# Performance work log

Measured on AMD Instinct MI355X. Metric: run time of the kernel, lower is better.

The kernel has to match this reference:

```python
import jax, jax.numpy as jnp
import numpy as np

B, T, C = 2, 2048, 2048
H, HK = 16, 4
HD = C // H
N_REP = H // HK


def setup_inputs() -> dict:
    key = jax.random.key(0)
    ks = jax.random.split(key, 10)
    sc_in = 1.0 / np.sqrt(C)
    x = jax.random.normal(ks[0], (B, T, C), dtype=jnp.float32)
    # rotary embeddings (realistic cos/sin from inv_freq)
    inv_freq = 1.0 / (10000.0 ** (jnp.arange(0, HD, 2, dtype=jnp.float32) / HD))
    freqs = jnp.arange(T, dtype=jnp.float32)[:, None] * inv_freq[None, :]  # [T, HD/2]
    emb = jnp.concatenate([freqs, freqs], axis=-1)  # [T, HD]
    cos = jnp.broadcast_to(jnp.cos(emb)[None], (B, T, HD))
    sin = jnp.broadcast_to(jnp.sin(emb)[None], (B, T, HD))
    Wq = jax.random.normal(ks[1], (C, H * HD), dtype=jnp.float32) * sc_in
    bq = jnp.zeros((H * HD,), dtype=jnp.float32)
    Wk = jax.random.normal(ks[2], (C, HK * HD), dtype=jnp.float32) * sc_in
    bk = jnp.zeros((HK * HD,), dtype=jnp.float32)
    Wv = jax.random.normal(ks[3], (C, HK * HD), dtype=jnp.float32) * sc_in
    bv = jnp.zeros((HK * HD,), dtype=jnp.float32)
    Wo = jax.random.normal(ks[4], (C, C), dtype=jnp.float32) * sc_in
    return {"x": x, "cos": cos, "sin": sin, "Wq": Wq, "bq": bq,
            "Wk": Wk, "bk": bk, "Wv": Wv, "bv": bv, "Wo": Wo}


def _rotate_half(t):
    t1, t2 = jnp.split(t, 2, axis=-1)
    return jnp.concatenate([-t2, t1], axis=-1)


def reference(x, cos, sin, Wq, bq, Wk, bk, Wv, bv, Wo):
    b, t, c = x.shape
    q = (x @ Wq + bq).reshape(b, t, H, HD).transpose(0, 2, 1, 3)   # [B,H,T,HD]
    k = (x @ Wk + bk).reshape(b, t, HK, HD).transpose(0, 2, 1, 3)  # [B,HK,T,HD]
    v = (x @ Wv + bv).reshape(b, t, HK, HD).transpose(0, 2, 1, 3)  # [B,HK,T,HD]
    co = cos[:, None, :, :]  # [B,1,T,HD]
    si = sin[:, None, :, :]
    q = q * co + _rotate_half(q) * si
    k = k * co + _rotate_half(k) * si
    # GQA without materializing repeated K/V: group query heads per KV head
    qg = q.reshape(b, HK, N_REP, t, HD)
    scale = 1.0 / np.sqrt(HD)
    scores = jnp.einsum('bgrqd,bgkd->bgrqk', qg, k) * scale  # [B,HK,n_rep,T,T]
    causal = jnp.tril(jnp.ones((t, t), dtype=bool))
    scores = jnp.where(causal, scores, jnp.finfo(scores.dtype).min)
    att = jax.nn.softmax(scores, axis=-1)
    yg = jnp.einsum('bgrqk,bgkd->bgrqd', att, v)  # [B,HK,n_rep,T,HD]
    y = yg.reshape(b, H, t, HD).transpose(0, 2, 1, 3).reshape(b, t, c)
    return y @ Wo
```

## Files before the change

kernel.cpp:

```cpp
#include <hip/hip_runtime.h>
#include <math.h>

#define BB 2
#define TT 2048
#define CC 2048
#define HH 16
#define HKK 4
#define HD 128
#define MM (BB*TT)

typedef short bf16x8 __attribute__((ext_vector_type(8)));
typedef float f32x4 __attribute__((ext_vector_type(4)));
typedef float f32x16 __attribute__((ext_vector_type(16)));
typedef int   i32x4 __attribute__((ext_vector_type(4)));

#define GLOBAL_AS(p) ((const __attribute__((address_space(1))) void*)(p))
#define LDS_AS(p)    ((__attribute__((address_space(3))) void*)(p))

__device__ __forceinline__ unsigned short f2bf(float f) {
    unsigned u = __float_as_uint(f);
    u += 0x7fff + ((u >> 16) & 1);
    return (unsigned short)(u >> 16);
}
__device__ __forceinline__ float bf2f(unsigned short h) {
    return __uint_as_float(((unsigned)h) << 16);
}

#define QSCALE (0.08838834764831845f * 1.44269504088896340736f)

__global__ __launch_bounds__(256) void prep_kernel(
    const float* __restrict__ x, const float* __restrict__ Wq,
    const float* __restrict__ Wk, const float* __restrict__ Wv,
    const float* __restrict__ Wo, unsigned short* __restrict__ xb,
    unsigned short* __restrict__ Wt, unsigned short* __restrict__ Wot)
{
    __shared__ float tile[64][65];
    int z = blockIdx.z;
    if (z >= 4) {
        int bid = (z - 4) * 1024 + blockIdx.y * 32 + blockIdx.x;
        size_t i = ((size_t)bid * 256 + threadIdx.x) * 8;
        float4 a = *(const float4*)&x[i];
        float4 b = *(const float4*)&x[i + 4];
        uint4 r;
        r.x = f2bf(a.x) | ((unsigned)f2bf(a.y) << 16);
        r.y = f2bf(a.z) | ((unsigned)f2bf(a.w) << 16);
        r.z = f2bf(b.x) | ((unsigned)f2bf(b.y) << 16);
        r.w = f2bf(b.z) | ((unsigned)f2bf(b.w) << 16);
        *(uint4*)&xb[i] = r;
        return;
    }
    const float* src; unsigned short* dst; int ldW, nmax, noff;
    if (z == 0)      { src = Wq; dst = Wt;  ldW = 2048; nmax = 2048; noff = 0; }
    else if (z == 1) { src = Wk; dst = Wt;  ldW = 512;  nmax = 512;  noff = 2048; }
    else if (z == 2) { src = Wv; dst = Wt;  ldW = 512;  nmax = 512;  noff = 2560; }
    else             { src = Wo; dst = Wot; ldW = 2048; nmax = 2048; noff = 0; }
    int n0 = blockIdx.y * 64;
    if (n0 >= nmax) return;
    int k0 = blockIdx.x * 64;
    int tx = threadIdx.x & 15, ty = threadIdx.x >> 4;
#pragma unroll
    for (int i = 0; i < 4; ++i) {
        int r = ty + i * 16;
        float4 v4 = *(const float4*)&src[(size_t)(k0 + r) * ldW + n0 + tx * 4];
        tile[r][tx * 4 + 0] = v4.x;
        tile[r][tx * 4 + 1] = v4.y;
        tile[r][tx * 4 + 2] = v4.z;
        tile[r][tx * 4 + 3] = v4.w;
    }
    __syncthreads();
#pragma unroll
    for (int i = 0; i < 4; ++i) {
        int r = ty + i * 16;
        int c = tx * 4;
        ushort4 o;
        o.x = f2bf(tile[c + 0][r]);
        o.y = f2bf(tile[c + 1][r]);
        o.z = f2bf(tile[c + 2][r]);
        o.w = f2bf(tile[c + 3][r]);
        *(ushort4*)&dst[(size_t)(noff + n0 + r) * 2048 + k0 + c] = o;
    }
}

__device__ __forceinline__ void gemm_core_128x128x64(
    const unsigned short* __restrict__ A, const unsigned short* __restrict__ B,
    short* As, short* Bs, int m0, int n0,
    const int* mrow, const int* nrow, f32x4 (&acc)[4][4])
{
    const int tid = threadIdx.x;
    const int lane = tid & 63;
    const int w = tid >> 6;
    const int lm = lane & 15;
    const int q8 = lane >> 4;
    const int lrow = lane >> 3;
    const int lchunk = lane & 7;

    for (int kt = 0; kt < CC; kt += 64) {
        __syncthreads();
#pragma unroll
        for (int jj = 0; jj < 4; ++jj) {
            int rA = w * 32 + jj * 8 + lrow;
            int cA = ((lchunk ^ (rA & 7)) << 3);
            __builtin_amdgcn_global_load_lds(
                GLOBAL_AS(&A[(size_t)(m0 + rA) * CC + kt + cA]),
                LDS_AS(&As[(w * 32 + jj * 8) * 64]), 16, 0, 0);
            __builtin_amdgcn_global_load_lds(
                GLOBAL_AS(&B[(size_t)(n0 + rA) * CC + kt + cA]),
                LDS_AS(&Bs[(w * 32 + jj * 8) * 64]), 16, 0, 0);
        }
        __syncthreads();
#pragma unroll
        for (int ksi = 0; ksi < 2; ++ksi) {
            bf16x8 af[4], bfr[4];
#pragma unroll
            for (int i = 0; i < 4; ++i) {
                int xo = (((ksi * 4 + q8) ^ (lm & 7)) << 3);
                af[i]  = *(const bf16x8*)&As[(mrow[i] + lm) * 64 + xo];
                bfr[i] = *(const bf16x8*)&Bs[(nrow[i] + lm) * 64 + xo];
            }
#pragma unroll
            for (int im = 0; im < 4; ++im)
#pragma unroll
                for (int in = 0; in < 4; ++in)
                    acc[im][in] = __builtin_amdgcn_mfma_f32_16x16x32_bf16(af[im], bfr[in], acc[im][in], 0, 0, 0);
        }
    }
}

__global__ __launch_bounds__(256, 3) void qkv_gemm_mfma(
    const unsigned short* __restrict__ xb, const unsigned short* __restrict__ Wt,
    const float* __restrict__ bq, const float* __restrict__ bk, const float* __restrict__ bv,
    const float* __restrict__ cosb, const float* __restrict__ sinb,
    unsigned short* __restrict__ q, unsigned short* __restrict__ k, unsigned short* __restrict__ v)
{
    __shared__ __attribute__((aligned(16))) short As[128 * 64];
    __shared__ __attribute__((aligned(16))) short Bs[128 * 64];
    const int lane = threadIdx.x & 63;
    const int w = threadIdx.x >> 6;
    const int w1 = w >> 1;
    const int m0 = blockIdx.y * 128;
    const int n0 = blockIdx.x * 128;
    const int lm = lane & 15;
    const int q8 = lane >> 4;

    int mrow[4], nrow[4];
#pragma unroll
    for (int i = 0; i < 4; ++i) {
        mrow[i] = (w & 1) * 64 + i * 16;
        nrow[i] = w1 * 32 + (i & 1) * 16 + (i >> 1) * 64;
    }

    f32x4 acc[4][4];
#pragma unroll
    for (int im = 0; im < 4; ++im)
#pragma unroll
        for (int in = 0; in < 4; ++in) acc[im][in] = {0.f, 0.f, 0.f, 0.f};

    gemm_core_128x128x64(xb, Wt, As, Bs, m0, n0, mrow, nrow, acc);

    unsigned short* dst; const float* bias; int ldD, off, mode;
    if (n0 < 2048)      { dst = q; bias = bq; ldD = 2048; off = n0;        mode = 0; }
    else if (n0 < 2560) { dst = k; bias = bk; ldD = 512;  off = n0 - 2048; mode = 1; }
    else                { dst = v; bias = bv; ldD = 512;  off = n0 - 2560; mode = 2; }

    float bv_[4];
#pragma unroll
    for (int in = 0; in < 4; ++in) bv_[in] = bias[off + nrow[in] + lm];

#pragma unroll
    for (int im = 0; im < 4; ++im) {
        int rowbase = m0 + mrow[im] + q8 * 4;
        float t[4][4];
#pragma unroll
        for (int in = 0; in < 4; ++in)
#pragma unroll
            for (int r = 0; r < 4; ++r) t[in][r] = acc[im][in][r] + bv_[in];
        if (mode < 2) {
#pragma unroll
            for (int in = 0; in < 4; ++in) {
                int d = nrow[in] + lm;
                float sgn = (in < 2) ? -1.f : 1.f;
#pragma unroll
                for (int r = 0; r < 4; ++r) {
                    int row = rowbase + r;
                    float c = cosb[row * HD + d];
                    float s = sinb[row * HD + d];
                    float o = c * t[in][r] + sgn * s * t[in ^ 2][r];
                    if (mode == 0) o *= QSCALE;
                    dst[(size_t)row * ldD + off + d] = f2bf(o);
                }
            }
        } else {
#pragma unroll
            for (int in = 0; in < 4; ++in)
#pragma unroll
                for (int r = 0; r < 4; ++r)
                    dst[(size_t)(rowbase + r) * ldD + off + nrow[in] + lm] = f2bf(t[in][r]);
        }
    }
}

__global__ __launch_bounds__(256, 3) void out_gemm_mfma(
    const unsigned short* __restrict__ yb, const unsigned short* __restrict__ Wot,
    float* __restrict__ Cout)
{
    __shared__ __attribute__((aligned(16))) short As[128 * 64];
    __shared__ __attribute__((aligned(16))) short Bs[128 * 64];
    const int lane = threadIdx.x & 63;
    const int w = threadIdx.x >> 6;
    const int m0 = blockIdx.y * 128;
    const int n0 = blockIdx.x * 128;
    const int lm = lane & 15;
    const int q8 = lane >> 4;

    int mrow[4], nrow[4];
#pragma unroll
    for (int i = 0; i < 4; ++i) {
        mrow[i] = (w & 1) * 64 + i * 16;
        nrow[i] = (w >> 1) * 64 + i * 16;
    }

    f32x4 acc[4][4];
#pragma unroll
    for (int im = 0; im < 4; ++im)
#pragma unroll
        for (int in = 0; in < 4; ++in) acc[im][in] = {0.f, 0.f, 0.f, 0.f};

    gemm_core_128x128x64(yb, Wot, As, Bs, m0, n0, mrow, nrow, acc);

#pragma unroll
    for (int im = 0; im < 4; ++im)
#pragma unroll
        for (int in = 0; in < 4; ++in)
#pragma unroll
            for (int r = 0; r < 4; ++r) {
                int row = m0 + mrow[im] + q8 * 4 + r;
                Cout[(size_t)row * CC + n0 + nrow[in] + lm] = acc[im][in][r];
            }
}

__global__ __launch_bounds__(256) void vtrans_kernel(
    const unsigned short* __restrict__ v, unsigned short* __restrict__ vt)
{
    __shared__ unsigned short tile[64][68];
    int bg = blockIdx.z;
    int b = bg >> 2, g = bg & 3;
    int t0 = blockIdx.x * 64;
    int d0 = blockIdx.y * 64;
    int tx = threadIdx.x & 15, ty = threadIdx.x >> 4;
#pragma unroll
    for (int i = 0; i < 4; ++i) {
        int r = ty + i * 16;
        ushort4 v4 = *(const ushort4*)&v[(size_t)(b * TT + t0 + r) * (HKK * HD) + g * HD + d0 + tx * 4];
        tile[r][tx * 4 + 0] = v4.x;
        tile[r][tx * 4 + 1] = v4.y;
        tile[r][tx * 4 + 2] = v4.z;
        tile[r][tx * 4 + 3] = v4.w;
    }
    __syncthreads();
#pragma unroll
    for (int i = 0; i < 4; ++i) {
        int r = ty + i * 16;
        int c = tx * 4;
        ushort4 o;
        o.x = tile[c + 0][r];
        o.y = tile[c + 1][r];
        o.z = tile[c + 2][r];
        o.w = tile[c + 3][r];
        *(ushort4*)&vt[(size_t)(bg * HD + d0 + r) * TT + t0 + c] = o;
    }
}

static __device__ const signed char QI_T[24] = {
    15, 7, 14, 14, 13, 6, 12, 11,
    15, 13, 12, 10, 10, 9, 11, 5,
    0, 1, 2, 3, 8, 4, 8, 9
};
static __device__ const signed char HF_T[24] = {
    0, 2, 0, 1, 1, 2, 1, 1,
    1, 0, 0, 0, 1, 0, 0, 2,
    2, 2, 2, 2, 0, 2, 1, 1
};

__global__ __launch_bounds__(256, 3) void flash_mfma(
    const unsigned short* __restrict__ q, const unsigned short* __restrict__ k,
    const unsigned short* __restrict__ vt, unsigned short* __restrict__ y,
    float* __restrict__ po, float* __restrict__ sb)
{
    __shared__ __attribute__((aligned(16))) short SM[24576];
    short* Vs = SM + 16384;

    const int tid = threadIdx.x;
    const int lane = tid & 63;
    const int w = tid >> 6;
    const int l31 = lane & 31;
    const int hi = lane >> 5;
    const int swz = (l31 & 7) << 3;
    const int bh = blockIdx.x;
    const int b = bh >> 4, h = bh & 15, g = h >> 2;
    const int yb_ = blockIdx.y;
    const int qi = QI_T[yb_];
    const int hf = HF_T[yb_];
    const int q0 = qi * 128;
    const int jdiag = 2 * qi + (w >> 1);
    int j0, jend;
    if (hf == 2)      { j0 = 0;      jend = 2 * qi + 2; }
    else if (hf == 0) { j0 = 0;      jend = qi + 1; }
    else              { j0 = qi + 1; jend = 2 * qi + 2; }

    bf16x8 qf[8];
#pragma unroll
    for (int ks = 0; ks < 8; ++ks)
        qf[ks] = *(const bf16x8*)&q[(size_t)(b * TT + q0 + w * 32 + l31) * CC
                                    + h * HD + ks * 16 + hi * 8];

    f32x16 o_acc[4];
#pragma unroll
    for (int t = 0; t < 4; ++t)
#pragma unroll
        for (int e = 0; e < 16; ++e) o_acc[t][e] = 0.f;
    float m_i = -1e30f;
    float l_i = 0.f;

    const unsigned short* kbase = k + (size_t)(b * TT) * (HKK * HD) + g * HD;
    const unsigned short* vbase = vt + (size_t)((b * 4 + g) * HD) * TT;
    int ko[4], vo[4];
#pragma unroll
    for (int i = 0; i < 4; ++i) {
        int c = (i * 4 + w) * 64 + lane;
        int kt_ = c >> 4, kc = c & 15;
        ko[i] = kt_ * (HKK * HD) + ((kc ^ (kt_ & 7)) << 3);
        int dv = c >> 3, vc = c & 7;
        vo[i] = dv * TT + ((vc ^ (dv & 7)) << 3);
    }

#define STAGE_K(cb, jj) do {                                                 \
    short* Kd = SM + (cb) * 8192;                                            \
    _Pragma("unroll")                                                        \
    for (int i_ = 0; i_ < 4; ++i_)                                           \
        __builtin_amdgcn_global_load_lds(                                    \
            GLOBAL_AS(kbase + (size_t)(jj) * 64 * (HKK * HD) + ko[i_]),      \
            LDS_AS(Kd + (i_ * 4 + w) * 512), 16, 0, 0);                      \
} while (0)
#define STAGE_V(jj) do {                                                     \
    _Pragma("unroll")                                                        \
    for (int i_ = 0; i_ < 4; ++i_)                                           \
        __builtin_amdgcn_global_load_lds(                                    \
            GLOBAL_AS(vbase + (size_t)(jj) * 64 + vo[i_]),                   \
            LDS_AS(Vs + (i_ * 4 + w) * 512), 16, 0, 0);                      \
} while (0)

    STAGE_K(0, j0);
    __syncthreads();

    int c = 0;
    for (int j = j0; j < jend; ++j) {
        STAGE_V(j);
        int jn = (j + 1 < jend) ? j + 1 : j;
        STAGE_K(c ^ 1, jn);

        f32x16 sacc[2];
        if (j <= jdiag) {
            const short* Ks = SM + c * 8192;
#pragma unroll
            for (int ct = 0; ct < 2; ++ct) {
#pragma unroll
                for (int e = 0; e < 16; ++e) sacc[ct][e] = 0.f;
#pragma unroll
                for (int ks = 0; ks < 8; ++ks) {
                    bf16x8 kf = *(const bf16x8*)&Ks[(ct * 32 + l31) * 128
                                                    + (((2 * ks + hi) << 3) ^ swz)];
                    sacc[ct] = __builtin_amdgcn_mfma_f32_32x32x16_bf16(kf, qf[ks], sacc[ct], 0, 0, 0);
                }
            }
            if (j == jdiag) {
                int lim = l31 + 32 * (w & 1);
#pragma unroll
                for (int ct = 0; ct < 2; ++ct)
#pragma unroll
                    for (int reg = 0; reg < 16; ++reg) {
                        int tok = ct * 32 + (reg & 3) + 8 * (reg >> 2) + 4 * hi;
                        if (tok > lim) sacc[ct][reg] = -1e30f;
                    }
            }
            float mx[8];
#pragma unroll
            for (int e = 0; e < 8; ++e)
                mx[e] = fmaxf(fmaxf(sacc[0][e], sacc[0][e + 8]),
                              fmaxf(sacc[1][e], sacc[1][e + 8]));
            float tmax = fmaxf(fmaxf(fmaxf(mx[0], mx[1]), fmaxf(mx[2], mx[3])),
                               fmaxf(fmaxf(mx[4], mx[5]), fmaxf(mx[6], mx[7])));
            tmax = fmaxf(tmax, __shfl_xor(tmax, 32));
            float m_new = fmaxf(m_i, tmax);
            float alpha = exp2f(m_i - m_new);
            m_i = m_new;

#pragma unroll
            for (int ct = 0; ct < 2; ++ct)
#pragma unroll
                for (int e = 0; e < 16; ++e)
                    sacc[ct][e] = exp2f(sacc[ct][e] - m_new);
            float s8[8];
#pragma unroll
            for (int e = 0; e < 8; ++e)
                s8[e] = (sacc[0][e] + sacc[0][e + 8]) + (sacc[1][e] + sacc[1][e + 8]);
            float ps = ((s8[0] + s8[1]) + (s8[2] + s8[3]))
                     + ((s8[4] + s8[5]) + (s8[6] + s8[7]));
            l_i = l_i * alpha + ps;

#pragma unroll
            for (int t = 0; t < 4; ++t)
#pragma unroll
                for (int e = 0; e < 16; ++e) o_acc[t][e] *= alpha;
        }

        asm volatile("s_waitcnt vmcnt(4)" ::: "memory");
        __builtin_amdgcn_sched_barrier(0);
        __builtin_amdgcn_s_barrier();
        __builtin_amdgcn_sched_barrier(0);

        if (j <= jdiag) {
#pragma unroll
            for (int ks = 0; ks < 4; ++ks) {
                const int ct = ks >> 1, base = 8 * (ks & 1);
                int a0, a1, b0, b1;
                asm("v_cvt_pk_bf16_f32 %0, %1, %2" : "=v"(a0)
                    : "v"(sacc[ct][base + 0]), "v"(sacc[ct][base + 1]));
                asm("v_cvt_pk_bf16_f32 %0, %1, %2" : "=v"(a1)
                    : "v"(sacc[ct][base + 2]), "v"(sacc[ct][base + 3]));
                asm("v_cvt_pk_bf16_f32 %0, %1, %2" : "=v"(b0)
                    : "v"(sacc[ct][base + 4]), "v"(sacc[ct][base + 5]));
                asm("v_cvt_pk_bf16_f32 %0, %1, %2" : "=v"(b1)
                    : "v"(sacc[ct][base + 6]), "v"(sacc[ct][base + 7]));
                asm("v_permlane32_swap_b32 %0, %1" : "+v"(a0), "+v"(b0));
                asm("v_permlane32_swap_b32 %0, %1" : "+v"(a1), "+v"(b1));
                i32x4 wv; wv[0] = a0; wv[1] = a1; wv[2] = b0; wv[3] = b1;
                bf16x8 pa = __builtin_bit_cast(bf16x8, wv);
#pragma unroll
                for (int t = 0; t < 4; ++t) {
                    bf16x8 vf = *(const bf16x8*)&Vs[(t * 32 + l31) * 64
                                                    + (((2 * ks + hi) << 3) ^ swz)];
                    o_acc[t] = __builtin_amdgcn_mfma_f32_32x32x16_bf16(vf, pa, o_acc[t], 0, 0, 0);
                }
            }
        }

        __syncthreads();
        c ^= 1;
    }
#undef STAGE_K
#undef STAGE_V

    float lf = l_i + __shfl_xor(l_i, 32);
    float invl = 1.f / lf;

    if (hf == 2) {
        short* Es = SM;
#pragma unroll
        for (int t = 0; t < 4; ++t)
#pragma unroll
            for (int rg = 0; rg < 4; ++rg) {
                ushort4 o;
                o.x = f2bf(o_acc[t][rg * 4 + 0] * invl);
                o.y = f2bf(o_acc[t][rg * 4 + 1] * invl);
                o.z = f2bf(o_acc[t][rg * 4 + 2] * invl);
                o.w = f2bf(o_acc[t][rg * 4 + 3] * invl);
                *(ushort4*)&Es[(w * 32 + l31) * 136 + t * 32 + 8 * rg + 4 * hi] = o;
            }
        __syncthreads();
#pragma unroll
        for (int i = 0; i < 8; ++i) {
            int f = tid + i * 256;
            int row = f >> 4, ch = f & 15;
            uint4 tv = *(const uint4*)&Es[row * 136 + ch * 8];
            *(uint4*)&y[(size_t)(b * TT + q0 + row) * CC + h * HD + ch * 8] = tv;
        }
    } else {
        const int pi = ((bh << 3) + (qi - 8)) * 2 + hf;
        if (hi == 0) sb[pi * 128 + w * 32 + l31] = lf * exp2f(m_i);
        float* pb = po + (size_t)pi * 16384;
#pragma unroll
        for (int t = 0; t < 4; ++t)
#pragma unroll
            for (int rg = 0; rg < 4; ++rg) {
                float4 o;
                o.x = o_acc[t][rg * 4 + 0] * invl;
                o.y = o_acc[t][rg * 4 + 1] * invl;
                o.z = o_acc[t][rg * 4 + 2] * invl;
                o.w = o_acc[t][rg * 4 + 3] * invl;
                *(float4*)&pb[(w * 32 + l31) * 128 + t * 32 + 8 * rg + 4 * hi] = o;
            }
    }
}

__global__ __launch_bounds__(256) void combine_kernel(
    const float* __restrict__ po, const float* __restrict__ sb,
    unsigned short* __restrict__ y)
{
    const int bh = blockIdx.x;
    const int b = bh >> 4, h = bh & 15;
    const int qi = 8 + blockIdx.y;
    const int p0 = ((bh << 3) + (qi - 8)) * 2;
    const int t = threadIdx.x;
    const int row = t >> 1, d0 = (t & 1) * 64;
    float s0 = sb[p0 * 128 + row];
    float s1 = sb[(p0 + 1) * 128 + row];
    float w0 = s0 / (s0 + s1);
    float w1 = 1.f - w0;
    const float* a = &po[(size_t)p0 * 16384 + row * 128 + d0];
    const float* c = &po[(size_t)(p0 + 1) * 16384 + row * 128 + d0];
    unsigned short* yr = &y[(size_t)(b * TT + qi * 128 + row) * CC + h * HD + d0];
#pragma unroll
    for (int i = 0; i < 64; i += 4) {
        float4 xa = *(const float4*)&a[i];
        float4 xc = *(const float4*)&c[i];
        ushort4 o;
        o.x = f2bf(w0 * xa.x + w1 * xc.x);
        o.y = f2bf(w0 * xa.y + w1 * xc.y);
        o.z = f2bf(w0 * xa.z + w1 * xc.z);
        o.w = f2bf(w0 * xa.w + w1 * xc.w);
        *(ushort4*)&yr[i] = o;
    }
}

extern "C" void kernel_launch(void* const* d_in, const int* in_sizes, int n_in,
                              void* d_out, int out_size, void* d_ws, size_t ws_size,
                              hipStream_t stream) {
    const float* x    = (const float*)d_in[0];
    const float* cosb = (const float*)d_in[1];
    const float* sinb = (const float*)d_in[2];
    const float* Wq   = (const float*)d_in[3];
    const float* bq   = (const float*)d_in[4];
    const float* Wk   = (const float*)d_in[5];
    const float* bk   = (const float*)d_in[6];
    const float* Wv   = (const float*)d_in[7];
    const float* bv   = (const float*)d_in[8];
    const float* Wo   = (const float*)d_in[9];
    float* out = (float*)d_out;

    unsigned short* xb  = (unsigned short*)d_ws;
    unsigned short* Wt  = xb  + (size_t)MM * CC;
    unsigned short* Wot = Wt  + (size_t)3072 * 2048;
    unsigned short* qb  = Wot + (size_t)2048 * 2048;
    unsigned short* kb  = qb  + (size_t)MM * CC;
    unsigned short* vb  = kb  + (size_t)MM * (HKK * HD);
    unsigned short* vtb = vb  + (size_t)MM * (HKK * HD);
    unsigned short* ybf = vtb + (size_t)BB * HKK * HD * TT;

    float* po = (float*)d_out;
    float* sbuf = (float*)xb;

    prep_kernel<<<dim3(32, 32, 8), 256, 0, stream>>>(x, Wq, Wk, Wv, Wo, xb, Wt, Wot);
    qkv_gemm_mfma<<<dim3(3072 / 128, MM / 128), 256, 0, stream>>>(
        xb, Wt, bq, bk, bv, cosb, sinb, qb, kb, vb);
    vtrans_kernel<<<dim3(TT / 64, HD / 64, BB * HKK), 256, 0, stream>>>(vb, vtb);
    flash_mfma<<<dim3(BB * HH, 24), 256, 0, stream>>>(qb, kb, vtb, ybf, po, sbuf);
    combine_kernel<<<dim3(BB * HH, 8), 256, 0, stream>>>(po, sbuf, ybf);
    out_gemm_mfma<<<dim3(CC / 128, MM / 128), 256, 0, stream>>>(ybf, Wot, out);
}
```

Measured before the change: 312.7 us.

## Fuse V transpose into QKV GEMM, swizzle GEMM blocks, lazy softmax rescale

The QKV GEMM epilogue for V tiles now transposes through LDS and writes the transposed V layout directly, so the separate vtrans kernel and its launch go away. Both GEMMs remap block indices with an XCD-aware swizzle to improve L2 locality. The flash kernel skips the running-max rescale of the output accumulator when the new tile max stays within a threshold of the old one (the FA4-style lazy rescale), and raises wave priority around the MFMA sections. The added LDS buffer for the transpose may reduce occupancy, and the lazy rescale lets exponentials exceed 1 by up to 2^8, which bounds their range but slightly changes numerics.

```diff
diff --git a/kernel.cpp b/kernel.cpp
--- a/kernel.cpp
+++ b/kernel.cpp
@@ -21,9 +21,6 @@
     unsigned u = __float_as_uint(f);
     u += 0x7fff + ((u >> 16) & 1);
     return (unsigned short)(u >> 16);
-}
-__device__ __forceinline__ float bf2f(unsigned short h) {
-    return __uint_as_float(((unsigned)h) << 16);
 }
 
 #define QSCALE (0.08838834764831845f * 1.44269504088896340736f)
@@ -130,15 +127,22 @@
     const unsigned short* __restrict__ xb, const unsigned short* __restrict__ Wt,
     const float* __restrict__ bq, const float* __restrict__ bk, const float* __restrict__ bv,
     const float* __restrict__ cosb, const float* __restrict__ sinb,
-    unsigned short* __restrict__ q, unsigned short* __restrict__ k, unsigned short* __restrict__ v)
+    unsigned short* __restrict__ q, unsigned short* __restrict__ k,
+    unsigned short* __restrict__ vt)
 {
-    __shared__ __attribute__((aligned(16))) short As[128 * 64];
-    __shared__ __attribute__((aligned(16))) short Bs[128 * 64];
-    const int lane = threadIdx.x & 63;
-    const int w = threadIdx.x >> 6;
+    __shared__ __attribute__((aligned(16))) short SM[17408];
+    short* As = SM;
+    short* Bs = SM + 8192;
+    const int tid = threadIdx.x;
+    const int lane = tid & 63;
+    const int w = tid >> 6;
     const int w1 = w >> 1;
-    const int m0 = blockIdx.y * 128;
-    const int n0 = blockIdx.x * 128;
+    const int nx = gridDim.x;
+    const int nwg = nx * gridDim.y;
+    const int bid = blockIdx.y * nx + blockIdx.x;
+    const int swb = (bid & 7) * (nwg >> 3) + (bid >> 3);
+    const int m0 = (swb / nx) * 128;
+    const int n0 = (swb % nx) * 128;
     const int lm = lane & 15;
     const int q8 = lane >> 4;
 
@@ -160,11 +164,47 @@
     unsigned short* dst; const float* bias; int ldD, off, mode;
     if (n0 < 2048)      { dst = q; bias = bq; ldD = 2048; off = n0;        mode = 0; }
     else if (n0 < 2560) { dst = k; bias = bk; ldD = 512;  off = n0 - 2048; mode = 1; }
-    else                { dst = v; bias = bv; ldD = 512;  off = n0 - 2560; mode = 2; }
+    else                { dst = 0; bias = bv; ldD = 0;    off = n0 - 2560; mode = 2; }
 
     float bv_[4];
 #pragma unroll
     for (int in = 0; in < 4; ++in) bv_[in] = bias[off + nrow[in] + lm];
+
+    if (mode == 2) {
+        __syncthreads();
+        short* Ts = SM;
+#pragma unroll
+        for (int im = 0; im < 4; ++im) {
+            int rowb = mrow[im] + q8 * 4;
+#pragma unroll
+            for (int in = 0; in < 4; ++in) {
+                float bvv = bv_[in];
+#pragma unroll
+                for (int r = 0; r < 4; ++r)
+                    Ts[(rowb + r) * 136 + nrow[in] + lm] =
+                        (short)f2bf(acc[im][in][r] + bvv);
+            }
+        }
+        __syncthreads();
+        int d = tid >> 1, th = (tid & 1) * 64;
+        int bb = m0 >> 11, t0 = m0 & 2047, gg = off >> 7;
+        unsigned short* vr = &vt[(size_t)((bb * 4 + gg) * HD + d) * TT + t0 + th];
+#pragma unroll
+        for (int i = 0; i < 8; ++i) {
+            int tb = th + i * 8;
+            unsigned o0 = (unsigned short)Ts[(tb + 0) * 136 + d]
+                        | ((unsigned)(unsigned short)Ts[(tb + 1) * 136 + d] << 16);
+            unsigned o1 = (unsigned short)Ts[(tb + 2) * 136 + d]
+                        | ((unsigned)(unsigned short)Ts[(tb + 3) * 136 + d] << 16);
+            unsigned o2 = (unsigned short)Ts[(tb + 4) * 136 + d]
+                        | ((unsigned)(unsigned short)Ts[(tb + 5) * 136 + d] << 16);
+            unsigned o3 = (unsigned short)Ts[(tb + 6) * 136 + d]
+                        | ((unsigned)(unsigned short)Ts[(tb + 7) * 136 + d] << 16);
+            uint4 o; o.x = o0; o.y = o1; o.z = o2; o.w = o3;
+            *(uint4*)&vr[i * 8] = o;
+        }
+        return;
+    }
 
 #pragma unroll
     for (int im = 0; im < 4; ++im) {
@@ -174,27 +214,19 @@
         for (int in = 0; in < 4; ++in)
 #pragma unroll
             for (int r = 0; r < 4; ++r) t[in][r] = acc[im][in][r] + bv_[in];
-        if (mode < 2) {
-#pragma unroll
-            for (int in = 0; in < 4; ++in) {
-                int d = nrow[in] + lm;
-                float sgn = (in < 2) ? -1.f : 1.f;
-#pragma unroll
-                for (int r = 0; r < 4; ++r) {
-                    int row = rowbase + r;
-                    float c = cosb[row * HD + d];
-                    float s = sinb[row * HD + d];
-                    float o = c * t[in][r] + sgn * s * t[in ^ 2][r];
-                    if (mode == 0) o *= QSCALE;
-                    dst[(size_t)row * ldD + off + d] = f2bf(o);
-                }
-            }
-        } else {
-#pragma unroll
-            for (int in = 0; in < 4; ++in)
-#pragma unroll
-                for (int r = 0; r < 4; ++r)
-                    dst[(size_t)(rowbase + r) * ldD + off + nrow[in] + lm] = f2bf(t[in][r]);
+#pragma unroll
+        for (int in = 0; in < 4; ++in) {
+            int d = nrow[in] + lm;
+            float sgn = (in < 2) ? -1.f : 1.f;
+#pragma unroll
+            for (int r = 0; r < 4; ++r) {
+                int row = rowbase + r;
+                float c = cosb[row * HD + d];
+                float s = sinb[row * HD + d];
+                float o = c * t[in][r] + sgn * s * t[in ^ 2][r];
+                if (mode == 0) o *= QSCALE;
+                dst[(size_t)row * ldD + off + d] = f2bf(o);
+            }
         }
     }
 }
@@ -207,8 +239,12 @@
     __shared__ __attribute__((aligned(16))) short Bs[128 * 64];
     const int lane = threadIdx.x & 63;
     const int w = threadIdx.x >> 6;
-    const int m0 = blockIdx.y * 128;
-    const int n0 = blockIdx.x * 128;
+    const int nx = gridDim.x;
+    const int nwg = nx * gridDim.y;
+    const int bid = blockIdx.y * nx + blockIdx.x;
+    const int swb = (bid & 7) * (nwg >> 3) + (bid >> 3);
+    const int m0 = (swb / nx) * 128;
+    const int n0 = (swb % nx) * 128;
     const int lm = lane & 15;
     const int q8 = lane >> 4;
 
@@ -236,38 +272,6 @@
                 int row = m0 + mrow[im] + q8 * 4 + r;
                 Cout[(size_t)row * CC + n0 + nrow[in] + lm] = acc[im][in][r];
             }
-}
-
-__global__ __launch_bounds__(256) void vtrans_kernel(
-    const unsigned short* __restrict__ v, unsigned short* __restrict__ vt)
-{
-    __shared__ unsigned short tile[64][68];
-    int bg = blockIdx.z;
-    int b = bg >> 2, g = bg & 3;
-    int t0 = blockIdx.x * 64;
-    int d0 = blockIdx.y * 64;
-    int tx = threadIdx.x & 15, ty = threadIdx.x >> 4;
-#pragma unroll
-    for (int i = 0; i < 4; ++i) {
-        int r = ty + i * 16;
-        ushort4 v4 = *(const ushort4*)&v[(size_t)(b * TT + t0 + r) * (HKK * HD) + g * HD + d0 + tx * 4];
-        tile[r][tx * 4 + 0] = v4.x;
-        tile[r][tx * 4 + 1] = v4.y;
-        tile[r][tx * 4 + 2] = v4.z;
-        tile[r][tx * 4 + 3] = v4.w;
-    }
-    __syncthreads();
-#pragma unroll
-    for (int i = 0; i < 4; ++i) {
-        int r = ty + i * 16;
-        int c = tx * 4;
-        ushort4 o;
-        o.x = tile[c + 0][r];
-        o.y = tile[c + 1][r];
-        o.z = tile[c + 2][r];
-        o.w = tile[c + 3][r];
-        *(ushort4*)&vt[(size_t)(bg * HD + d0 + r) * TT + t0 + c] = o;
-    }
 }
 
 static __device__ const signed char QI_T[24] = {
@@ -361,6 +365,7 @@
         f32x16 sacc[2];
         if (j <= jdiag) {
             const short* Ks = SM + c * 8192;
+            __builtin_amdgcn_s_setprio(1);
 #pragma unroll
             for (int ct = 0; ct < 2; ++ct) {
 #pragma unroll
@@ -372,6 +377,7 @@
                     sacc[ct] = __builtin_amdgcn_mfma_f32_32x32x16_bf16(kf, qf[ks], sacc[ct], 0, 0, 0);
                 }
             }
+            __builtin_amdgcn_s_setprio(0);
             if (j == jdiag) {
                 int lim = l31 + 32 * (w & 1);
 #pragma unroll
@@ -390,27 +396,30 @@
             float tmax = fmaxf(fmaxf(fmaxf(mx[0], mx[1]), fmaxf(mx[2], mx[3])),
                                fmaxf(fmaxf(mx[4], mx[5]), fmaxf(mx[6], mx[7])));
             tmax = fmaxf(tmax, __shfl_xor(tmax, 32));
-            float m_new = fmaxf(m_i, tmax);
-            float alpha = exp2f(m_i - m_new);
-            m_i = m_new;
+
+            if (!__all(tmax <= m_i + 8.0f)) {
+                float m_new = fmaxf(m_i, tmax);
+                float alpha = exp2f(m_i - m_new);
+                m_i = m_new;
+                l_i *= alpha;
+#pragma unroll
+                for (int t = 0; t < 4; ++t)
+#pragma unroll
+                    for (int e = 0; e < 16; ++e) o_acc[t][e] *= alpha;
+            }
 
 #pragma unroll
             for (int ct = 0; ct < 2; ++ct)
 #pragma unroll
                 for (int e = 0; e < 16; ++e)
-                    sacc[ct][e] = exp2f(sacc[ct][e] - m_new);
+                    sacc[ct][e] = exp2f(sacc[ct][e] - m_i);
             float s8[8];
 #pragma unroll
             for (int e = 0; e < 8; ++e)
                 s8[e] = (sacc[0][e] + sacc[0][e + 8]) + (sacc[1][e] + sacc[1][e + 8]);
             float ps = ((s8[0] + s8[1]) + (s8[2] + s8[3]))
                      + ((s8[4] + s8[5]) + (s8[6] + s8[7]));
-            l_i = l_i * alpha + ps;
-
-#pragma unroll
-            for (int t = 0; t < 4; ++t)
-#pragma unroll
-                for (int e = 0; e < 16; ++e) o_acc[t][e] *= alpha;
+            l_i += ps;
         }
 
         asm volatile("s_waitcnt vmcnt(4)" ::: "memory");
@@ -419,6 +428,7 @@
         __builtin_amdgcn_sched_barrier(0);
 
         if (j <= jdiag) {
+            __builtin_amdgcn_s_setprio(1);
 #pragma unroll
             for (int ks = 0; ks < 4; ++ks) {
                 const int ct = ks >> 1, base = 8 * (ks & 1);
@@ -442,6 +452,7 @@
                     o_acc[t] = __builtin_amdgcn_mfma_f32_32x32x16_bf16(vf, pa, o_acc[t], 0, 0, 0);
                 }
             }
+            __builtin_amdgcn_s_setprio(0);
         }
 
         __syncthreads();
@@ -551,8 +562,7 @@
 
     prep_kernel<<<dim3(32, 32, 8), 256, 0, stream>>>(x, Wq, Wk, Wv, Wo, xb, Wt, Wot);
     qkv_gemm_mfma<<<dim3(3072 / 128, MM / 128), 256, 0, stream>>>(
-        xb, Wt, bq, bk, bv, cosb, sinb, qb, kb, vb);
-    vtrans_kernel<<<dim3(TT / 64, HD / 64, BB * HKK), 256, 0, stream>>>(vb, vtb);
+        xb, Wt, bq, bk, bv, cosb, sinb, qb, kb, vtb);
     flash_mfma<<<dim3(BB * HH, 24), 256, 0, stream>>>(qb, kb, vtb, ybf, po, sbuf);
     combine_kernel<<<dim3(BB * HH, 8), 256, 0, stream>>>(po, sbuf, ybf);
     out_gemm_mfma<<<dim3(CC / 128, MM / 128), 256, 0, stream>>>(ybf, Wot, out);
```

Measured after the change: 313.0 us. Within noise of the previous version (+0.1%).
